# Optimization experiments

Measured on AMD Instinct MI355X. Metric: run time of the kernel, lower is better.

The kernel has to match this reference:

```python
import jax, jax.numpy as jnp
import numpy as np
from jax import lax

BT, ST, NT = 32, 8, 1024
CH = [128, 64, 32, 16, 8]
DIL = [1, 2, 4, 8, 16]
K = 5
EPS = 1e-5


def setup_inputs() -> dict:
    key = jax.random.key(0)
    ks = jax.random.split(key, 32)
    inp = {}
    inp["x"] = jax.random.normal(ks[0], (BT, ST, CH[0], NT), jnp.float32)
    nt_out = NT * 32  # 5 x2 upsamples
    inp["targets"] = jax.random.uniform(ks[1], (BT, 3, nt_out, ST), dtype=jnp.float32)
    for i in range(4):
        inp[f"w{i}"] = jax.random.normal(ks[2 + i], (CH[i + 1], CH[i], K), jnp.float32) * 0.05
        inp[f"g{i}"] = 1.0 + 0.1 * jax.random.normal(ks[6 + i], (CH[i + 1],), jnp.float32)
        inp[f"b{i}"] = 0.1 * jax.random.normal(ks[10 + i], (CH[i + 1],), jnp.float32)
        inp[f"m{i}"] = 0.1 * jax.random.normal(ks[14 + i], (CH[i + 1],), jnp.float32)
        inp[f"v{i}"] = 0.5 + 0.5 * jax.random.uniform(ks[18 + i], (CH[i + 1],), dtype=jnp.float32)
    inp["w_out"] = jax.random.normal(ks[22], (3, CH[4], K), jnp.float32) * 0.05
    inp["b_out"] = jax.random.normal(ks[23], (3,), jnp.float32) * 0.05
    return inp


def _conv(x, w, d):
    # reflect-padded dilated conv1d, same length out (torch padding_mode='reflect')
    p = ((K - 1) * d + 1) // 2
    xp = jnp.pad(x, ((0, 0), (0, 0), (p, p)), mode="reflect")
    return lax.conv_general_dilated(xp, w, window_strides=(1,), padding="VALID",
                                    rhs_dilation=(d,),
                                    dimension_numbers=("NCH", "OIH", "NCH"))


def _up2(x):
    # F.interpolate(scale_factor=2, mode='linear', align_corners=False)
    L = x.shape[-1]
    coords = (jnp.arange(2 * L, dtype=jnp.float32) + 0.5) / 2.0 - 0.5
    coords = jnp.clip(coords, 0.0, L - 1.0)
    i0 = jnp.floor(coords).astype(jnp.int32)
    i1 = jnp.minimum(i0 + 1, L - 1)
    w = coords - i0.astype(jnp.float32)
    return x[..., i0] * (1.0 - w) + x[..., i1] * w


def _forward(x, targets, ws, gs, bs, ms, vs, w_out, b_out):
    h = x.reshape(BT * ST, CH[0], NT)
    for i in range(4):
        h = _conv(h, ws[i], DIL[i])
        inv = gs[i] / jnp.sqrt(vs[i] + EPS)
        h = h * inv[None, :, None] + (bs[i] - ms[i] * inv)[None, :, None]  # eval-mode BN
        h = jax.nn.relu(h)
        h = _up2(h)
    h = _conv(h, w_out, DIL[4]) + b_out[None, :, None]
    h = _up2(h)
    out = h.reshape(BT, ST, 3, h.shape[-1]).transpose(0, 2, 3, 1)  # [bt, 3, nt_out, st]
    # vectorized equivalent of the per-(i,j) Python loop counting non-all-zero targets
    mask = jnp.any(targets != 0, axis=(1, 2))  # [bt, st]
    num = jnp.sum(mask).astype(jnp.float32)
    loss = jnp.sum(-targets * jax.nn.log_softmax(out, axis=1)) / (num * targets.shape[2])
    return out, loss


def reference(x, targets, w0, w1, w2, w3, g0, g1, g2, g3, b0, b1, b2, b3,
              m0, m1, m2, m3, v0, v1, v2, v3, w_out, b_out):
    return _forward(x, targets, [w0, w1, w2, w3], [g0, g1, g2, g3],
                    [b0, b1, b2, b3], [m0, m1, m2, m3], [v0, v1, v2, v3],
                    w_out, b_out)
```

## Files before the change

### kernel.cpp

```cpp
#include <hip/hip_runtime.h>
#include <hip/hip_bf16.h>
#include <cstdint>
#include <cstddef>

#define K5 5
#define BNEPS 1e-5f

typedef __attribute__((ext_vector_type(8))) short short8v;
typedef __attribute__((ext_vector_type(4))) float float4v;

template<int CIN, int COUT, int MROWS, int KPAD>
__global__ __launch_bounds__(256) void wprep2_ker(const float* __restrict__ w,
                                                  short* __restrict__ wb) {
    int idx = blockIdx.x * 256 + threadIdx.x;
    if (idx >= MROWS * KPAD) return;
    int co = idx / KPAD, kk = idx - co * KPAD;
    int tap = kk / CIN, ci = kk & (CIN - 1);
    float v = (co < COUT && tap < K5) ? w[((size_t)co * CIN + ci) * K5 + tap] : 0.f;
    __hip_bfloat16 h = __float2bfloat16(v);
    wb[idx] = *(short*)&h;
}

template<int CIN, int COUT, int DIL, int LOUT, bool UP_IN, int T_TILE, int WT,
         bool HAS_BN>
__global__ __launch_bounds__(256) void conv_mfma2_ker(
    const float* __restrict__ in, const short* __restrict__ wb,
    const float* __restrict__ gg, const float* __restrict__ bb,
    const float* __restrict__ mm, const float* __restrict__ vv,
    float* __restrict__ out)
{
    constexpr int P = 2 * DIL;
    constexpr int XT = T_TILE + 4 * DIL;
    constexpr int ROWW = CIN + 8;
    constexpr int K = CIN * K5;
    constexpr int KPAD = ((K + 31) / 32) * 32;
    constexpr int NSTEP = KPAD / 32;
    constexpr int MT = (COUT + 15) / 16;
    constexpr int WCOT = MT;
    constexpr int TN = T_TILE / (16 * WT);
    constexpr int LIN = LOUT;
    constexpr int LIN_BASE = UP_IN ? (LOUT / 2) : LOUT;

    __shared__ short sx[XT * ROWW];
    __shared__ float ssc[COUT], ssh[COUT];

    const int n = blockIdx.x;
    const int t0 = blockIdx.y * T_TILE;
    const int tid = threadIdx.x;

    if (tid < COUT) {
        if constexpr (HAS_BN) {
            float inv = gg[tid] * rsqrtf(vv[tid] + BNEPS);
            ssc[tid] = inv;
            ssh[tid] = bb[tid] - mm[tid] * inv;
        } else {
            ssc[tid] = 1.f;
            ssh[tid] = bb[tid];
        }
    }

    for (int uidx = tid; uidx < XT * (CIN / 8); uidx += 256) {
        int t = uidx % XT;
        int ci0 = (uidx / XT) * 8;
        int u = t0 - P + t;
        u = (u < 0) ? -u : u;
        u = (u >= LIN) ? (2 * (LIN - 1) - u) : u;
        const float* base = in + ((size_t)n * CIN + ci0) * LIN_BASE;
        short8v pack;
        if constexpr (UP_IN) {
            int i = u >> 1;
            int ia, ib; float wa, wbw;
            if (u & 1) { ia = i; ib = (i + 1 < LIN_BASE) ? i + 1 : LIN_BASE - 1; wa = 0.75f; wbw = 0.25f; }
            else if (i == 0) { ia = 0; ib = 0; wa = 1.0f; wbw = 0.0f; }
            else { ia = i - 1; ib = i; wa = 0.25f; wbw = 0.75f; }
#pragma unroll
            for (int j = 0; j < 8; ++j) {
                float v = wa * base[(size_t)j * LIN_BASE + ia] + wbw * base[(size_t)j * LIN_BASE + ib];
                __hip_bfloat16 h = __float2bfloat16(v);
                pack[j] = *(short*)&h;
            }
        } else {
#pragma unroll
            for (int j = 0; j < 8; ++j) {
                __hip_bfloat16 h = __float2bfloat16(base[(size_t)j * LIN_BASE + u]);
                pack[j] = *(short*)&h;
            }
        }
        *(short8v*)(sx + t * ROWW + ci0) = pack;
    }
    __syncthreads();

    const int wvi = tid >> 6;
    const int lane = tid & 63;
    const int ln = lane & 15;
    const int q = lane >> 4;
    const int tw = wvi * (TN * 16);

    float4v acc[WCOT][TN];
#pragma unroll
    for (int c = 0; c < WCOT; ++c)
#pragma unroll
        for (int j = 0; j < TN; ++j)
            acc[c][j] = (float4v){0.f, 0.f, 0.f, 0.f};

    const short* arow[WCOT];
#pragma unroll
    for (int c = 0; c < WCOT; ++c)
        arow[c] = wb + ((size_t)(c * 16 + ln)) * KPAD + q * 8;

    short8v acur[WCOT], anx[WCOT];
#pragma unroll
    for (int c = 0; c < WCOT; ++c)
        acur[c] = *(const short8v*)(arow[c]);

#pragma unroll 1
    for (int s = 0; s < NSTEP; ++s) {
        if (s + 1 < NSTEP) {
#pragma unroll
            for (int c = 0; c < WCOT; ++c)
                anx[c] = *(const short8v*)(arow[c] + (s + 1) * 32);
        }
        const int kk = s * 32 + q * 8;
        int tap = kk / CIN;
        const int ci0 = kk & (CIN - 1);
        if constexpr (KPAD != K) {
            tap = (tap < K5) ? tap : (K5 - 1);
        }
        short8v b[TN];
#pragma unroll
        for (int j = 0; j < TN; ++j)
            b[j] = *(const short8v*)(sx + (tw + j * 16 + ln + tap * DIL) * ROWW + ci0);
        if constexpr (KPAD != K) {
            if (kk >= K) {
                short8v z = {0, 0, 0, 0, 0, 0, 0, 0};
#pragma unroll
                for (int j = 0; j < TN; ++j) b[j] = z;
            }
        }
#pragma unroll
        for (int c = 0; c < WCOT; ++c)
#pragma unroll
            for (int j = 0; j < TN; ++j)
                acc[c][j] = __builtin_amdgcn_mfma_f32_16x16x32_bf16(acur[c], b[j], acc[c][j], 0, 0, 0);
#pragma unroll
        for (int c = 0; c < WCOT; ++c)
            acur[c] = anx[c];
    }

    float* ob = out + (size_t)n * COUT * LOUT + t0 + tw + ln;
#pragma unroll
    for (int c = 0; c < WCOT; ++c)
#pragma unroll
        for (int j = 0; j < TN; ++j) {
            float4v v = acc[c][j];
#pragma unroll
            for (int r = 0; r < 4; ++r) {
                int co = c * 16 + q * 4 + r;
                if ((COUT % 16 == 0) || co < COUT) {
                    float val = v[r] * ssc[co] + ssh[co];
                    if constexpr (HAS_BN) val = fmaxf(val, 0.f);
                    ob[(size_t)co * LOUT + j * 16] = val;
                }
            }
        }
}

__global__ __launch_bounds__(256) void up_loss_ker(
    const float* __restrict__ h4, const float* __restrict__ targets,
    float* __restrict__ out, float* __restrict__ loss_sum, int* __restrict__ flags)
{
    constexpr int L = 16384, LO = 32768;
    const int bt = blockIdx.x;
    const int t0 = blockIdx.y * 256;
    const int tid = threadIdx.x;
    const int st = tid & 7, tloc = tid >> 3;
    const int i0 = t0 >> 1;

    __shared__ float sh[3 * 8 * 132];
    __shared__ int snz[8];
    __shared__ float swv[4];

    for (int idx = tid; idx < 3 * 8 * 132; idx += 256) {
        int row = idx / 132;
        int j = idx - row * 132;
        int c = row >> 3, s = row & 7;
        int bi = i0 - 1 + j;
        bi = bi < 0 ? 0 : (bi > L - 1 ? L - 1 : bi);
        int n = bt * 8 + s;
        sh[idx] = h4[((size_t)n * 3 + c) * L + bi];
    }
    if (tid < 8) snz[tid] = 0;
    __syncthreads();

    float lsum = 0.f;
    int nz = 0;
#pragma unroll
    for (int r = 0; r < 8; ++r) {
        int t = t0 + r * 32 + tloc;
        float o[3], tg[3];
        int i = t >> 1;
        int li = i - i0 + 1;
#pragma unroll
        for (int c = 0; c < 3; ++c) {
            const float* row = sh + (c * 8 + st) * 132;
            float v;
            if (t & 1) v = 0.75f * row[li] + 0.25f * row[li + 1];
            else       v = 0.25f * row[li - 1] + 0.75f * row[li];
            o[c] = v;
            size_t oidx = (((size_t)bt * 3 + c) * LO + t) * 8 + st;
            out[oidx] = v;
            tg[c] = targets[oidx];
        }
        float mx = fmaxf(o[0], fmaxf(o[1], o[2]));
        float e0 = __expf(o[0] - mx), e1 = __expf(o[1] - mx), e2 = __expf(o[2] - mx);
        float lse = mx + __logf(e0 + e1 + e2);
        lsum += tg[0] * (lse - o[0]) + tg[1] * (lse - o[1]) + tg[2] * (lse - o[2]);
        nz |= (tg[0] != 0.f) | (tg[1] != 0.f) | (tg[2] != 0.f);
    }
    if (nz) snz[st] = 1;

#pragma unroll
    for (int off = 32; off > 0; off >>= 1) lsum += __shfl_down(lsum, off, 64);
    if ((tid & 63) == 0) swv[tid >> 6] = lsum;
    __syncthreads();
    if (tid == 0) atomicAdd(loss_sum, swv[0] + swv[1] + swv[2] + swv[3]);
    if (tid < 8 && snz[tid]) atomicOr(&flags[bt * 8 + tid], 1);
}

__global__ __launch_bounds__(256) void finalize_ker(
    const int* __restrict__ flags, const float* __restrict__ loss_sum,
    float* __restrict__ out_loss)
{
    __shared__ int s[256];
    s[threadIdx.x] = flags[threadIdx.x] ? 1 : 0;
    __syncthreads();
    for (int off = 128; off > 0; off >>= 1) {
        if (threadIdx.x < off) s[threadIdx.x] += s[threadIdx.x + off];
        __syncthreads();
    }
    if (threadIdx.x == 0) out_loss[0] = loss_sum[0] / ((float)s[0] * 32768.0f);
}

extern "C" void kernel_launch(void* const* d_in, const int* in_sizes, int n_in,
                              void* d_out, int out_size, void* d_ws, size_t ws_size,
                              hipStream_t stream)
{
    const float* x  = (const float*)d_in[0];
    const float* tg = (const float*)d_in[1];
    const float* w0 = (const float*)d_in[2];
    const float* g0 = (const float*)d_in[3];
    const float* b0 = (const float*)d_in[4];
    const float* m0 = (const float*)d_in[5];
    const float* v0 = (const float*)d_in[6];
    const float* w1 = (const float*)d_in[7];
    const float* g1 = (const float*)d_in[8];
    const float* b1 = (const float*)d_in[9];
    const float* m1 = (const float*)d_in[10];
    const float* v1 = (const float*)d_in[11];
    const float* w2 = (const float*)d_in[12];
    const float* g2 = (const float*)d_in[13];
    const float* b2 = (const float*)d_in[14];
    const float* m2 = (const float*)d_in[15];
    const float* v2 = (const float*)d_in[16];
    const float* w3 = (const float*)d_in[17];
    const float* g3 = (const float*)d_in[18];
    const float* b3 = (const float*)d_in[19];
    const float* m3 = (const float*)d_in[20];
    const float* v3 = (const float*)d_in[21];
    const float* w_out = (const float*)d_in[22];
    const float* b_out = (const float*)d_in[23];
    float* outp = (float*)d_out;

    char* ws = (char*)d_ws;
    int* flags = (int*)ws;
    float* loss_sum = (float*)(ws + 1024);
    short* wb0 = (short*)(ws + 4096);
    short* wb1 = (short*)(ws + 86016);
    short* wb2 = (short*)(ws + 106496);
    short* wb3 = (short*)(ws + 111616);
    short* wb4 = (short*)(ws + 114688);
    const size_t BUF_OFF = 131072;
    const size_t BUFN = (size_t)16777216;
    float* bufA = (float*)(ws + BUF_OFF);
    float* bufB = (ws_size >= BUF_OFF + 2 * BUFN * 4)
                      ? (bufA + BUFN)
                      : (float*)d_out;

    hipMemsetAsync(d_ws, 0, 4096, stream);

    wprep2_ker<128, 64, 64, 640><<<160, 256, 0, stream>>>(w0, wb0);
    wprep2_ker<64, 32, 32, 320><<<40, 256, 0, stream>>>(w1, wb1);
    wprep2_ker<32, 16, 16, 160><<<10, 256, 0, stream>>>(w2, wb2);
    wprep2_ker<16, 8, 16, 96><<<6, 256, 0, stream>>>(w3, wb3);
    wprep2_ker<8, 3, 16, 64><<<4, 256, 0, stream>>>(w_out, wb4);

    conv_mfma2_ker<128, 64, 1, 1024, false, 128, 4, true>
        <<<dim3(256, 8), 256, 0, stream>>>(x, wb0, g0, b0, m0, v0, bufA);
    conv_mfma2_ker<64, 32, 2, 2048, true, 128, 4, true>
        <<<dim3(256, 16), 256, 0, stream>>>(bufA, wb1, g1, b1, m1, v1, bufB);
    conv_mfma2_ker<32, 16, 4, 4096, true, 256, 4, true>
        <<<dim3(256, 16), 256, 0, stream>>>(bufB, wb2, g2, b2, m2, v2, bufA);
    conv_mfma2_ker<16, 8, 8, 8192, true, 256, 4, true>
        <<<dim3(256, 32), 256, 0, stream>>>(bufA, wb3, g3, b3, m3, v3, bufB);
    conv_mfma2_ker<8, 3, 16, 16384, true, 256, 4, false>
        <<<dim3(256, 64), 256, 0, stream>>>(bufB, wb4, b_out, b_out, b_out, b_out, bufA);
    up_loss_ker<<<dim3(32, 128), 256, 0, stream>>>(bufA, tg, outp, loss_sum, flags);
    finalize_ker<<<1, 256, 0, stream>>>(flags, loss_sum, outp + (size_t)(out_size - 1));
}
```

Before: 591.6 us.

## Vectorize conv input staging and loss kernel, merge weight prep, tune tiles

Conv input staging now has each thread handle four consecutive time positions, loading float4 vectors (computing the x2 linear upsample from them in registers) on an interior fast path, with a scalar reflect-padded fallback at the edges. The loss kernel loads its shared tile with float4 reads and writes outputs and reads targets four stations at a time. The five weight-prep launches are merged into one kernel, the first conv's time tile is halved so it launches twice as many blocks, and per-kernel occupancy hints are added to launch bounds. The intent is fewer, wider memory transactions and less launch overhead, at the cost of more register pressure and unaligned vector loads.

```diff
diff --git a/kernel.cpp b/kernel.cpp
--- a/kernel.cpp
+++ b/kernel.cpp
@@ -9,10 +9,12 @@
 typedef __attribute__((ext_vector_type(8))) short short8v;
 typedef __attribute__((ext_vector_type(4))) float float4v;
 
+struct __attribute__((packed, aligned(4))) f4u { float4v v; };
+
 template<int CIN, int COUT, int MROWS, int KPAD>
-__global__ __launch_bounds__(256) void wprep2_ker(const float* __restrict__ w,
-                                                  short* __restrict__ wb) {
-    int idx = blockIdx.x * 256 + threadIdx.x;
+__device__ inline void wprep_body(const float* __restrict__ w,
+                                  short* __restrict__ wb, int blk, int tid) {
+    int idx = blk * 256 + tid;
     if (idx >= MROWS * KPAD) return;
     int co = idx / KPAD, kk = idx - co * KPAD;
     int tap = kk / CIN, ci = kk & (CIN - 1);
@@ -21,9 +23,23 @@
     wb[idx] = *(short*)&h;
 }
 
+__global__ __launch_bounds__(256) void wprep_all_ker(
+    const float* __restrict__ w0, const float* __restrict__ w1,
+    const float* __restrict__ w2, const float* __restrict__ w3,
+    const float* __restrict__ w4,
+    short* __restrict__ wb0, short* __restrict__ wb1, short* __restrict__ wb2,
+    short* __restrict__ wb3, short* __restrict__ wb4) {
+    int b = blockIdx.x, t = threadIdx.x;
+    if (b < 160)      wprep_body<128, 64, 64, 640>(w0, wb0, b, t);
+    else if (b < 200) wprep_body<64, 32, 32, 320>(w1, wb1, b - 160, t);
+    else if (b < 210) wprep_body<32, 16, 16, 160>(w2, wb2, b - 200, t);
+    else if (b < 216) wprep_body<16, 8, 16, 96>(w3, wb3, b - 210, t);
+    else              wprep_body<8, 3, 16, 64>(w4, wb4, b - 216, t);
+}
+
 template<int CIN, int COUT, int DIL, int LOUT, bool UP_IN, int T_TILE, int WT,
-         bool HAS_BN>
-__global__ __launch_bounds__(256) void conv_mfma2_ker(
+         bool HAS_BN, int MW>
+__global__ __launch_bounds__(256, MW) void conv_mfma2_ker(
     const float* __restrict__ in, const short* __restrict__ wb,
     const float* __restrict__ gg, const float* __restrict__ bb,
     const float* __restrict__ mm, const float* __restrict__ vv,
@@ -40,6 +56,10 @@
     constexpr int TN = T_TILE / (16 * WT);
     constexpr int LIN = LOUT;
     constexpr int LIN_BASE = UP_IN ? (LOUT / 2) : LOUT;
+    static_assert(XT % 4 == 0, "XT must be multiple of 4");
+    static_assert(T_TILE % (16 * WT) == 0, "tile split");
+    constexpr int T4 = XT / 4;
+    constexpr int NITEM = T4 * (CIN / 8);
 
     __shared__ short sx[XT * ROWW];
     __shared__ float ssc[COUT], ssh[COUT];
@@ -59,34 +79,75 @@
         }
     }
 
-    for (int uidx = tid; uidx < XT * (CIN / 8); uidx += 256) {
-        int t = uidx % XT;
-        int ci0 = (uidx / XT) * 8;
-        int u = t0 - P + t;
-        u = (u < 0) ? -u : u;
-        u = (u >= LIN) ? (2 * (LIN - 1) - u) : u;
+    for (int uidx = tid; uidx < NITEM; uidx += 256) {
+        int t4 = uidx % T4;
+        int ci0 = (uidx / T4) * 8;
+        const int u0 = t0 - P + 4 * t4;
         const float* base = in + ((size_t)n * CIN + ci0) * LIN_BASE;
-        short8v pack;
-        if constexpr (UP_IN) {
-            int i = u >> 1;
-            int ia, ib; float wa, wbw;
-            if (u & 1) { ia = i; ib = (i + 1 < LIN_BASE) ? i + 1 : LIN_BASE - 1; wa = 0.75f; wbw = 0.25f; }
-            else if (i == 0) { ia = 0; ib = 0; wa = 1.0f; wbw = 0.0f; }
-            else { ia = i - 1; ib = i; wa = 0.25f; wbw = 0.75f; }
-#pragma unroll
-            for (int j = 0; j < 8; ++j) {
-                float v = wa * base[(size_t)j * LIN_BASE + ia] + wbw * base[(size_t)j * LIN_BASE + ib];
-                __hip_bfloat16 h = __float2bfloat16(v);
-                pack[j] = *(short*)&h;
+        short8v rows[4];
+        bool fast;
+        if constexpr (UP_IN) fast = (u0 >= 2) && (u0 <= LIN - 6);
+        else                 fast = (u0 >= 0) && (u0 + 3 <= LIN - 1);
+        if (fast) {
+            if constexpr (UP_IN) {
+                const int m = u0 >> 1;
+#pragma unroll
+                for (int j = 0; j < 8; ++j) {
+                    f4u xv = *(const f4u*)(base + (size_t)j * LIN_BASE + (m - 1));
+                    float o0 = 0.25f * xv.v[0] + 0.75f * xv.v[1];
+                    float o1 = 0.75f * xv.v[1] + 0.25f * xv.v[2];
+                    float o2 = 0.25f * xv.v[1] + 0.75f * xv.v[2];
+                    float o3 = 0.75f * xv.v[2] + 0.25f * xv.v[3];
+                    __hip_bfloat16 ha = __float2bfloat16(o0);
+                    __hip_bfloat16 hb = __float2bfloat16(o1);
+                    __hip_bfloat16 hc = __float2bfloat16(o2);
+                    __hip_bfloat16 hd = __float2bfloat16(o3);
+                    rows[0][j] = *(short*)&ha; rows[1][j] = *(short*)&hb;
+                    rows[2][j] = *(short*)&hc; rows[3][j] = *(short*)&hd;
+                }
+            } else {
+#pragma unroll
+                for (int j = 0; j < 8; ++j) {
+                    f4u xv = *(const f4u*)(base + (size_t)j * LIN_BASE + u0);
+#pragma unroll
+                    for (int r = 0; r < 4; ++r) {
+                        __hip_bfloat16 hh = __float2bfloat16(xv.v[r]);
+                        rows[r][j] = *(short*)&hh;
+                    }
+                }
             }
         } else {
 #pragma unroll
-            for (int j = 0; j < 8; ++j) {
-                __hip_bfloat16 h = __float2bfloat16(base[(size_t)j * LIN_BASE + u]);
-                pack[j] = *(short*)&h;
-            }
-        }
-        *(short8v*)(sx + t * ROWW + ci0) = pack;
+            for (int r = 0; r < 4; ++r) {
+                int u = u0 + r;
+                u = (u < 0) ? -u : u;
+                u = (u >= LIN) ? (2 * (LIN - 1) - u) : u;
+                if constexpr (UP_IN) {
+                    int i = u >> 1;
+                    int ia, ib; float wa, wbw;
+                    if (u & 1) { ia = i; ib = (i + 1 < LIN_BASE) ? i + 1 : LIN_BASE - 1; wa = 0.75f; wbw = 0.25f; }
+                    else if (i == 0) { ia = 0; ib = 0; wa = 1.0f; wbw = 0.0f; }
+                    else { ia = i - 1; ib = i; wa = 0.25f; wbw = 0.75f; }
+#pragma unroll
+                    for (int j = 0; j < 8; ++j) {
+                        float v = wa * base[(size_t)j * LIN_BASE + ia] + wbw * base[(size_t)j * LIN_BASE + ib];
+                        __hip_bfloat16 hh = __float2bfloat16(v);
+                        rows[r][j] = *(short*)&hh;
+                    }
+                } else {
+#pragma unroll
+                    for (int j = 0; j < 8; ++j) {
+                        __hip_bfloat16 hh = __float2bfloat16(base[(size_t)j * LIN_BASE + u]);
+                        rows[r][j] = *(short*)&hh;
+                    }
+                }
+            }
+        }
+        short* dst = sx + (4 * t4) * ROWW + ci0;
+        *(short8v*)(dst) = rows[0];
+        *(short8v*)(dst + ROWW) = rows[1];
+        *(short8v*)(dst + 2 * ROWW) = rows[2];
+        *(short8v*)(dst + 3 * ROWW) = rows[3];
     }
     __syncthreads();
 
@@ -173,51 +234,81 @@
     const int bt = blockIdx.x;
     const int t0 = blockIdx.y * 256;
     const int tid = threadIdx.x;
-    const int st = tid & 7, tloc = tid >> 3;
     const int i0 = t0 >> 1;
 
     __shared__ float sh[3 * 8 * 132];
     __shared__ int snz[8];
     __shared__ float swv[4];
 
-    for (int idx = tid; idx < 3 * 8 * 132; idx += 256) {
-        int row = idx / 132;
-        int j = idx - row * 132;
-        int c = row >> 3, s = row & 7;
-        int bi = i0 - 1 + j;
-        bi = bi < 0 ? 0 : (bi > L - 1 ? L - 1 : bi);
-        int n = bt * 8 + s;
-        sh[idx] = h4[((size_t)n * 3 + c) * L + bi];
+    {
+        const bool interior = (i0 >= 1) && (i0 + 130 <= L - 1);
+        for (int idx = tid; idx < 24 * 33; idx += 256) {
+            int row = idx / 33;
+            int qd = idx - row * 33;
+            int c = row >> 3, s = row & 7;
+            int nn = bt * 8 + s;
+            const float* src = h4 + ((size_t)nn * 3 + c) * L;
+            int bi0 = i0 - 1 + 4 * qd;
+            float4v v;
+            if (interior) {
+                v = ((const f4u*)(src + bi0))->v;
+            } else {
+#pragma unroll
+                for (int k = 0; k < 4; ++k) {
+                    int bi = bi0 + k;
+                    bi = bi < 0 ? 0 : (bi > L - 1 ? L - 1 : bi);
+                    v[k] = src[bi];
+                }
+            }
+            *(float4v*)(sh + row * 132 + 4 * qd) = v;
+        }
     }
     if (tid < 8) snz[tid] = 0;
     __syncthreads();
 
+    const int tl = tid >> 1;
+    const int st4 = (tid & 1) * 4;
+
     float lsum = 0.f;
-    int nz = 0;
-#pragma unroll
-    for (int r = 0; r < 8; ++r) {
-        int t = t0 + r * 32 + tloc;
-        float o[3], tg[3];
-        int i = t >> 1;
-        int li = i - i0 + 1;
+    int nzm = 0;
+#pragma unroll
+    for (int rr = 0; rr < 2; ++rr) {
+        int t = t0 + rr * 128 + tl;
+        int li = (t >> 1) - i0 + 1;
+        float o[3][4];
+#pragma unroll
+        for (int c = 0; c < 3; ++c)
+#pragma unroll
+            for (int s = 0; s < 4; ++s) {
+                const float* row = sh + ((c << 3) + st4 + s) * 132;
+                float v;
+                if (t & 1) v = 0.75f * row[li] + 0.25f * row[li + 1];
+                else       v = 0.25f * row[li - 1] + 0.75f * row[li];
+                o[c][s] = v;
+            }
+        float tg[3][4];
 #pragma unroll
         for (int c = 0; c < 3; ++c) {
-            const float* row = sh + (c * 8 + st) * 132;
-            float v;
-            if (t & 1) v = 0.75f * row[li] + 0.25f * row[li + 1];
-            else       v = 0.25f * row[li - 1] + 0.75f * row[li];
-            o[c] = v;
-            size_t oidx = (((size_t)bt * 3 + c) * LO + t) * 8 + st;
-            out[oidx] = v;
-            tg[c] = targets[oidx];
-        }
-        float mx = fmaxf(o[0], fmaxf(o[1], o[2]));
-        float e0 = __expf(o[0] - mx), e1 = __expf(o[1] - mx), e2 = __expf(o[2] - mx);
-        float lse = mx + __logf(e0 + e1 + e2);
-        lsum += tg[0] * (lse - o[0]) + tg[1] * (lse - o[1]) + tg[2] * (lse - o[2]);
-        nz |= (tg[0] != 0.f) | (tg[1] != 0.f) | (tg[2] != 0.f);
-    }
-    if (nz) snz[st] = 1;
+            size_t obase = (((size_t)bt * 3 + c) * LO + t) * 8 + st4;
+            float4v ov = { o[c][0], o[c][1], o[c][2], o[c][3] };
+            *(float4v*)(out + obase) = ov;
+            float4v tv = *(const float4v*)(targets + obase);
+            tg[c][0] = tv[0]; tg[c][1] = tv[1]; tg[c][2] = tv[2]; tg[c][3] = tv[3];
+        }
+#pragma unroll
+        for (int s = 0; s < 4; ++s) {
+            float a0 = o[0][s], a1 = o[1][s], a2 = o[2][s];
+            float mx = fmaxf(a0, fmaxf(a1, a2));
+            float e0 = __expf(a0 - mx), e1 = __expf(a1 - mx), e2 = __expf(a2 - mx);
+            float lse = mx + __logf(e0 + e1 + e2);
+            lsum += tg[0][s] * (lse - a0) + tg[1][s] * (lse - a1) + tg[2][s] * (lse - a2);
+            if ((tg[0][s] != 0.f) | (tg[1][s] != 0.f) | (tg[2][s] != 0.f)) nzm |= 1 << s;
+        }
+    }
+    if (nzm) {
+#pragma unroll
+        for (int s = 0; s < 4; ++s) if (nzm & (1 << s)) snz[st4 + s] = 1;
+    }
 
 #pragma unroll
     for (int off = 32; off > 0; off >>= 1) lsum += __shfl_down(lsum, off, 64);
@@ -288,21 +379,18 @@
 
     hipMemsetAsync(d_ws, 0, 4096, stream);
 
-    wprep2_ker<128, 64, 64, 640><<<160, 256, 0, stream>>>(w0, wb0);
-    wprep2_ker<64, 32, 32, 320><<<40, 256, 0, stream>>>(w1, wb1);
-    wprep2_ker<32, 16, 16, 160><<<10, 256, 0, stream>>>(w2, wb2);
-    wprep2_ker<16, 8, 16, 96><<<6, 256, 0, stream>>>(w3, wb3);
-    wprep2_ker<8, 3, 16, 64><<<4, 256, 0, stream>>>(w_out, wb4);
-
-    conv_mfma2_ker<128, 64, 1, 1024, false, 128, 4, true>
-        <<<dim3(256, 8), 256, 0, stream>>>(x, wb0, g0, b0, m0, v0, bufA);
-    conv_mfma2_ker<64, 32, 2, 2048, true, 128, 4, true>
+    wprep_all_ker<<<220, 256, 0, stream>>>(w0, w1, w2, w3, w_out,
+                                           wb0, wb1, wb2, wb3, wb4);
+
+    conv_mfma2_ker<128, 64, 1, 1024, false, 64, 4, true, 6>
+        <<<dim3(256, 16), 256, 0, stream>>>(x, wb0, g0, b0, m0, v0, bufA);
+    conv_mfma2_ker<64, 32, 2, 2048, true, 128, 4, true, 6>
         <<<dim3(256, 16), 256, 0, stream>>>(bufA, wb1, g1, b1, m1, v1, bufB);
-    conv_mfma2_ker<32, 16, 4, 4096, true, 256, 4, true>
+    conv_mfma2_ker<32, 16, 4, 4096, true, 256, 4, true, 8>
         <<<dim3(256, 16), 256, 0, stream>>>(bufB, wb2, g2, b2, m2, v2, bufA);
-    conv_mfma2_ker<16, 8, 8, 8192, true, 256, 4, true>
+    conv_mfma2_ker<16, 8, 8, 8192, true, 256, 4, true, 8>
         <<<dim3(256, 32), 256, 0, stream>>>(bufA, wb3, g3, b3, m3, v3, bufB);
-    conv_mfma2_ker<8, 3, 16, 16384, true, 256, 4, false>
+    conv_mfma2_ker<8, 3, 16, 16384, true, 256, 4, false, 8>
         <<<dim3(256, 64), 256, 0, stream>>>(bufB, wb4, b_out, b_out, b_out, b_out, bufA);
     up_loss_ker<<<dim3(32, 128), 256, 0, stream>>>(bufA, tg, outp, loss_sum, flags);
     finalize_ker<<<1, 256, 0, stream>>>(flags, loss_sum, outp + (size_t)(out_size - 1));
```

Result: slower. 659.5 us (+11.5%).
